# Kernel optimization log

Measured on AMD Instinct MI355X. Metric: run time of the kernel, lower is better.

Reference implementation:

```python
import jax, jax.numpy as jnp
import numpy as np

jax.config.update("jax_enable_x64", True)

P = 2038074743          # prime used by the ROBE-Z hash
BLOCK_K = 32            # tile sizes of the hashed reconstruction (kernel tile)
BLOCK_N = 32
INPUT_DIM = 8192
OUTPUT_DIM = 8192
HASH_SIZE = 1 << 22     # compressed parameter count
TOKENS = 512


def setup_inputs() -> dict:
    key = jax.random.key(0)
    k1, k2 = jax.random.split(key, 2)
    x = jax.random.normal(k1, (TOKENS, INPUT_DIM), dtype=jnp.float32)
    hashed_weight = jax.random.normal(k2, (HASH_SIZE,), dtype=jnp.float32) * 0.02
    bias = jnp.zeros((OUTPUT_DIM,), dtype=jnp.float32)
    # mirrors RzLinear._generate_random_numbers(seed): 4 random ints made even, prepended with P
    rng = np.random.RandomState(1024)
    r = rng.randint(0, P, size=(4,)).astype(np.int64)
    r = r + (r % 2)
    random_numbers = jnp.asarray(np.concatenate([np.array([P], dtype=np.int64), r]), dtype=jnp.int64)
    return {"x": x, "hashed_weight": hashed_weight, "bias": bias, "random_numbers": random_numbers}


def _weight_indices(random_numbers):
    """Hashed flat indices into hashed_weight for the dense [K, N] weight."""
    K, N = INPUT_DIM, OUTPUT_DIM
    kt, nt = K // BLOCK_K, N // BLOCK_N
    R1, R2, R3 = random_numbers[1], random_numbers[2], random_numbers[3]
    k_ids = jnp.arange(kt, dtype=jnp.int64)
    n_ids = jnp.arange(nt, dtype=jnp.int64)
    # per-tile start offset into the compressed array
    start = ((k_ids[:, None] * R3 + n_ids[None, :] * R2 + R1) % P) % (HASH_SIZE - BLOCK_K * BLOCK_N + 1)
    start = start.astype(jnp.int32)  # [kt, nt]
    off = (jnp.arange(BLOCK_K, dtype=jnp.int32)[:, None] * BLOCK_N
           + jnp.arange(BLOCK_N, dtype=jnp.int32)[None, :])  # [BK, BN], row-major within tile
    idx = start[:, None, :, None] + off[None, :, None, :]    # [kt, BK, nt, BN]
    return idx.reshape(K, N)


def reference(x, hashed_weight, bias, random_numbers):
    idx = _weight_indices(random_numbers)          # [K, N] int32
    W = hashed_weight[idx]                          # hashed-gather reconstruction, [K, N]
    out = jnp.matmul(x, W) + bias[None, :]          # [tokens, N]
    return out
```

## Files before the change

### kernel.cpp

```cpp
#include <hip/hip_runtime.h>
#include <hip/hip_fp16.h>

#define NDIM 8192
#define KDIM 8192
#define NT 256
#define MOD2 4193281
#define PRIME 2038074743LL

#define BM 256
#define BN 128
#define BK 32
#define KITER 64
#define BSLAB 1032

typedef _Float16 half8 __attribute__((ext_vector_type(8)));
typedef float floatx4 __attribute__((ext_vector_type(4)));

__global__ __launch_bounds__(256) void prep_kernel(const float* __restrict__ x,
                                                   const float* __restrict__ hw,
                                                   const float* __restrict__ bias,
                                                   const int* __restrict__ rn,
                                                   __half* __restrict__ xh,
                                                   __half* __restrict__ hh,
                                                   int* __restrict__ starts,
                                                   float* __restrict__ out) {
    int b = blockIdx.x;
    int tid = threadIdx.x;
    if (b < 8192) {
        int i = b * 256 + tid;
        const float4* s; __half2* d; int j;
        if (i < (1 << 20)) { s = (const float4*)x;  d = (__half2*)xh; j = i; }
        else               { s = (const float4*)hw; d = (__half2*)hh; j = i - (1 << 20); }
        float4 v = s[j];
        d[j * 2]     = __floats2half2_rn(v.x, v.y);
        d[j * 2 + 1] = __floats2half2_rn(v.z, v.w);
    } else if (b < 8192 + 4096) {
        int i = (b - 8192) * 256 + tid;
        float4 bv = *(const float4*)(bias + ((i & 2047) << 2));
        ((float4*)out)[i] = bv;
    } else {
        int t = (b - 12288) * 256 + tid;
        bool is64 = (rn[1] == 0 && rn[3] == 0);
        long long R1 = is64 ? rn[2] : rn[1];
        long long R2 = is64 ? rn[4] : rn[2];
        long long R3 = is64 ? rn[6] : rn[3];
        long long k_id = t >> 8, n_id = t & 255;
        long long v = (k_id * R3 + n_id * R2 + R1) % PRIME;
        starts[t] = (int)(v % MOD2);
    }
}

__device__ __forceinline__ void gload16(const __half* g, __half* l) {
    __builtin_amdgcn_global_load_lds((const __attribute__((address_space(1))) void*)g,
                                     (__attribute__((address_space(3))) void*)l, 16, 0, 0);
}

#define SBAR() __builtin_amdgcn_sched_barrier(0)
#define WAIT_LGKM0() __builtin_amdgcn_s_waitcnt(0xC07F)

__global__ __launch_bounds__(512, 4) void gemm_kernel(
    const __half* __restrict__ xh, const __half* __restrict__ hh,
    const int* __restrict__ starts, float* __restrict__ out) {
    __shared__ __align__(16) __half As[3][BM * 32];
    __shared__ __align__(16) __half Bs[3][4 * BSLAB];
    __shared__ int Ss[KITER * 4];

    const int tid = threadIdx.x;
    const int lane = tid & 63;
    const int wave = tid >> 6;
    const int wm = wave >> 1;
    const int wn = wave & 1;
    const int quad = lane >> 4;
    const int l16 = lane & 15;

    const int i = blockIdx.x;
    const int ks = i & 3;
    const int m_blk = (i >> 2) & 1;
    const int n_blk = i >> 3;
    const int gm0 = m_blk * BM;
    const int gn0 = n_blk * BN;
    const int kt0 = ks * KITER;
    const int n_id0 = n_blk * 4;

    if (tid < KITER * 4) {
        int kp = tid >> 2, tile = tid & 3;
        Ss[tid] = starts[(kt0 + kp) * NT + n_id0 + tile];
    }

    const int a_t = wave * 2;
    const int a_chunk = (lane & 3) ^ ((lane >> 3) & 3);
    const __half* a_g0 = xh + (size_t)(gm0 + a_t * 16 + (lane >> 2)) * KDIM
                         + kt0 * 32 + a_chunk * 8;
    const __half* a_g1 = a_g0 + (size_t)16 * KDIM;

#define STAGE_A(c_, kp_) do {                                                  \
        gload16(a_g0 + (kp_) * 32, &As[c_][a_t * 512]);                        \
        gload16(a_g1 + (kp_) * 32, &As[c_][a_t * 512 + 512]);                  \
    } while (0)

    const int b_tile = tid >> 7;
    const int t7 = tid & 127;
    const int b_np = t7 & 15;
    const int b_kg = t7 >> 4;
    const int b_oct = b_kg >> 1;
    const unsigned b_base = b_oct * BSLAB;
    const unsigned b_pos = (b_tile * 32 + 2 * b_np) * 8 + (b_kg & 1) * 4;
    const unsigned bswz = (b_np & 4) << 1;

    unsigned pbA0, pbA1, pbA2, pbA3, pbB0, pbB1, pbB2, pbB3;

#define LOADT(Q0, Q1, Q2, Q3, kp_) do {                                        \
        int st = Ss[(kp_) * 4 + b_tile];                                       \
        const __half* src = hh + st + b_kg * 128 + b_np * 2;                   \
        Q0 = *(const unsigned*)(src);                                          \
        Q1 = *(const unsigned*)(src + 32);                                     \
        Q2 = *(const unsigned*)(src + 64);                                     \
        Q3 = *(const unsigned*)(src + 96);                                     \
    } while (0)

#define STORET(Q0, Q1, Q2, Q3, c_) do {                                        \
        unsigned lo0 = (Q0 & 0xffffu) | (Q1 << 16);                            \
        unsigned lo1 = (Q2 & 0xffffu) | (Q3 << 16);                            \
        unsigned hi0 = (Q0 >> 16) | (Q1 & 0xffff0000u);                        \
        unsigned hi1 = (Q2 >> 16) | (Q3 & 0xffff0000u);                        \
        uint2 e = {lo0, lo1}, o = {hi0, hi1};                                  \
        *(uint2*)&Bs[c_][b_base + (b_pos ^ bswz)] = e;                         \
        *(uint2*)&Bs[c_][b_base + ((b_pos + 8) ^ bswz)] = o;                   \
    } while (0)

    floatx4 acc[4][4];
#pragma unroll
    for (int r = 0; r < 4; r++)
#pragma unroll
        for (int c = 0; c < 4; c++)
            acc[r][c] = (floatx4){0.f, 0.f, 0.f, 0.f};

    const unsigned rswz = (unsigned)(l16 & 8);
    const unsigned a_rswz = (unsigned)((l16 >> 1) & 3);

    half8 fa0, fa1, fa2, fa3, fb0, fb1, fb2, fb3;

#define READF(c_) do {                                                         \
        fa0 = *(const half8*)&As[c_][(unsigned)(wm * 64 +  0 + l16) * 32 + ((quad ^ a_rswz) * 8)]; \
        fa1 = *(const half8*)&As[c_][(unsigned)(wm * 64 + 16 + l16) * 32 + ((quad ^ a_rswz) * 8)]; \
        fa2 = *(const half8*)&As[c_][(unsigned)(wm * 64 + 32 + l16) * 32 + ((quad ^ a_rswz) * 8)]; \
        fa3 = *(const half8*)&As[c_][(unsigned)(wm * 64 + 48 + l16) * 32 + ((quad ^ a_rswz) * 8)]; \
        fb0 = *(const half8*)&Bs[c_][quad * BSLAB + ((unsigned)((wn * 64 +  0 + l16) * 8) ^ rswz)]; \
        fb1 = *(const half8*)&Bs[c_][quad * BSLAB + ((unsigned)((wn * 64 + 16 + l16) * 8) ^ rswz)]; \
        fb2 = *(const half8*)&Bs[c_][quad * BSLAB + ((unsigned)((wn * 64 + 32 + l16) * 8) ^ rswz)]; \
        fb3 = *(const half8*)&Bs[c_][quad * BSLAB + ((unsigned)((wn * 64 + 48 + l16) * 8) ^ rswz)]; \
    } while (0)

#define MFMAC() do {                                                           \
        __builtin_amdgcn_s_setprio(1);                                         \
        acc[0][0] = __builtin_amdgcn_mfma_f32_16x16x32_f16(fa0, fb0, acc[0][0], 0, 0, 0); \
        acc[1][0] = __builtin_amdgcn_mfma_f32_16x16x32_f16(fa1, fb0, acc[1][0], 0, 0, 0); \
        acc[2][0] = __builtin_amdgcn_mfma_f32_16x16x32_f16(fa2, fb0, acc[2][0], 0, 0, 0); \
        acc[3][0] = __builtin_amdgcn_mfma_f32_16x16x32_f16(fa3, fb0, acc[3][0], 0, 0, 0); \
        acc[0][1] = __builtin_amdgcn_mfma_f32_16x16x32_f16(fa0, fb1, acc[0][1], 0, 0, 0); \
        acc[1][1] = __builtin_amdgcn_mfma_f32_16x16x32_f16(fa1, fb1, acc[1][1], 0, 0, 0); \
        acc[2][1] = __builtin_amdgcn_mfma_f32_16x16x32_f16(fa2, fb1, acc[2][1], 0, 0, 0); \
        acc[3][1] = __builtin_amdgcn_mfma_f32_16x16x32_f16(fa3, fb1, acc[3][1], 0, 0, 0); \
        acc[0][2] = __builtin_amdgcn_mfma_f32_16x16x32_f16(fa0, fb2, acc[0][2], 0, 0, 0); \
        acc[1][2] = __builtin_amdgcn_mfma_f32_16x16x32_f16(fa1, fb2, acc[1][2], 0, 0, 0); \
        acc[2][2] = __builtin_amdgcn_mfma_f32_16x16x32_f16(fa2, fb2, acc[2][2], 0, 0, 0); \
        acc[3][2] = __builtin_amdgcn_mfma_f32_16x16x32_f16(fa3, fb2, acc[3][2], 0, 0, 0); \
        acc[0][3] = __builtin_amdgcn_mfma_f32_16x16x32_f16(fa0, fb3, acc[0][3], 0, 0, 0); \
        acc[1][3] = __builtin_amdgcn_mfma_f32_16x16x32_f16(fa1, fb3, acc[1][3], 0, 0, 0); \
        acc[2][3] = __builtin_amdgcn_mfma_f32_16x16x32_f16(fa2, fb3, acc[2][3], 0, 0, 0); \
        acc[3][3] = __builtin_amdgcn_mfma_f32_16x16x32_f16(fa3, fb3, acc[3][3], 0, 0, 0); \
        __builtin_amdgcn_s_setprio(0);                                         \
    } while (0)

    unsigned ca = 0, cb = 1, cc = 2, ct;
#define ROT() do { ct = ca; ca = cb; cb = cc; cc = ct; } while (0)

    __syncthreads();
    STAGE_A(0, 0);
    SBAR();
    LOADT(pbA0, pbA1, pbA2, pbA3, 0);
    STAGE_A(1, 1);
    SBAR();
    LOADT(pbB0, pbB1, pbB2, pbB3, 1);
    STORET(pbA0, pbA1, pbA2, pbA3, 0);
    __syncthreads();

    for (int kp = 0; kp < KITER; kp += 2) {
        READF(ca);
        if (kp + 2 < KITER) {
            STAGE_A(cc, kp + 2);
            SBAR();
            LOADT(pbA0, pbA1, pbA2, pbA3, kp + 2);
        }
        SBAR();
        __builtin_amdgcn_s_barrier();
        SBAR();
        MFMAC();
        STORET(pbB0, pbB1, pbB2, pbB3, cb);
        SBAR();
        WAIT_LGKM0();
        __builtin_amdgcn_s_barrier();
        SBAR();
        ROT();

        READF(ca);
        if (kp + 3 < KITER) {
            STAGE_A(cc, kp + 3);
            SBAR();
            LOADT(pbB0, pbB1, pbB2, pbB3, kp + 3);
        }
        SBAR();
        __builtin_amdgcn_s_barrier();
        SBAR();
        MFMAC();
        if (kp + 2 < KITER)
            STORET(pbA0, pbA1, pbA2, pbA3, cb);
        SBAR();
        WAIT_LGKM0();
        __builtin_amdgcn_s_barrier();
        SBAR();
        ROT();
    }

#pragma unroll
    for (int c = 0; c < 4; c++) {
        int col = gn0 + wn * 64 + c * 16 + l16;
#pragma unroll
        for (int r = 0; r < 4; r++) {
            int row0 = gm0 + wm * 64 + r * 16 + quad * 4;
#pragma unroll
            for (int e = 0; e < 4; e++)
                atomicAdd(&out[(size_t)(row0 + e) * NDIM + col], acc[r][c][e]);
        }
    }
#undef LOADT
#undef STORET
#undef READF
#undef MFMAC
#undef STAGE_A
#undef ROT
}

extern "C" void kernel_launch(void* const* d_in, const int* in_sizes, int n_in,
                              void* d_out, int out_size, void* d_ws, size_t ws_size,
                              hipStream_t stream) {
    const float* x = (const float*)d_in[0];
    const float* hw = (const float*)d_in[1];
    const float* bias = (const float*)d_in[2];
    const int* rn = (const int*)d_in[3];
    float* out = (float*)d_out;

    char* ws = (char*)d_ws;
    __half* xh = (__half*)ws;
    __half* hh = (__half*)(ws + (8u << 20));
    int* starts = (int*)(ws + (16u << 20));

    hipLaunchKernelGGL(prep_kernel, dim3(12544), dim3(256), 0, stream,
                       x, hw, bias, rn, xh, hh, starts, out);
    hipLaunchKernelGGL(gemm_kernel, dim3(512), dim3(512), 0, stream, xh, hh, starts, out);
}
```

Before: 195.7 us.

## Deepen GEMM K-loop pipeline to one barrier per stage with static buffer indices

Reworks the main K loop from a rotating triple-buffer with two barriers per step into an unrolled six-phase schedule. Each phase reads fragments from one LDS buffer, stages A and loads B tiles further ahead, waits once on LDS, barriers once, then issues the MFMAs and stores the B tile. A prologue and explicit epilogue are added. The goal is to halve barrier count and keep more global loads in flight. The cost is longer register lifetimes, more code, and tighter correctness requirements on hazards between buffers.

```diff
diff --git a/kernel.cpp b/kernel.cpp
--- a/kernel.cpp
+++ b/kernel.cpp
@@ -172,55 +172,63 @@
         __builtin_amdgcn_s_setprio(0);                                         \
     } while (0)
 
-    unsigned ca = 0, cb = 1, cc = 2, ct;
-#define ROT() do { ct = ca; ca = cb; cb = cc; cc = ct; } while (0)
+#define PHASE(bR, bS, QL0,QL1,QL2,QL3, QS0,QS1,QS2,QS3, t_) do {               \
+        READF(bR);                                                             \
+        STAGE_A(bS, (t_) + 2);                                                 \
+        SBAR();                                                                \
+        LOADT(QL0,QL1,QL2,QL3, (t_) + 3);                                      \
+        SBAR();                                                                \
+        WAIT_LGKM0();                                                          \
+        __builtin_amdgcn_s_barrier();                                          \
+        SBAR();                                                                \
+        MFMAC();                                                               \
+        STORET(QS0,QS1,QS2,QS3, bS);                                           \
+        SBAR();                                                                \
+    } while (0)
 
     __syncthreads();
     STAGE_A(0, 0);
+    STAGE_A(1, 1);
     SBAR();
     LOADT(pbA0, pbA1, pbA2, pbA3, 0);
-    STAGE_A(1, 1);
-    SBAR();
     LOADT(pbB0, pbB1, pbB2, pbB3, 1);
     STORET(pbA0, pbA1, pbA2, pbA3, 0);
+    SBAR();
+    LOADT(pbA0, pbA1, pbA2, pbA3, 2);
+    STORET(pbB0, pbB1, pbB2, pbB3, 1);
     __syncthreads();
 
-    for (int kp = 0; kp < KITER; kp += 2) {
-        READF(ca);
-        if (kp + 2 < KITER) {
-            STAGE_A(cc, kp + 2);
-            SBAR();
-            LOADT(pbA0, pbA1, pbA2, pbA3, kp + 2);
-        }
-        SBAR();
-        __builtin_amdgcn_s_barrier();
-        SBAR();
-        MFMAC();
-        STORET(pbB0, pbB1, pbB2, pbB3, cb);
-        SBAR();
-        WAIT_LGKM0();
-        __builtin_amdgcn_s_barrier();
-        SBAR();
-        ROT();
-
-        READF(ca);
-        if (kp + 3 < KITER) {
-            STAGE_A(cc, kp + 3);
-            SBAR();
-            LOADT(pbB0, pbB1, pbB2, pbB3, kp + 3);
-        }
-        SBAR();
-        __builtin_amdgcn_s_barrier();
-        SBAR();
-        MFMAC();
-        if (kp + 2 < KITER)
-            STORET(pbA0, pbA1, pbA2, pbA3, cb);
-        SBAR();
-        WAIT_LGKM0();
-        __builtin_amdgcn_s_barrier();
-        SBAR();
-        ROT();
-    }
+    for (int t = 0; t < 60; t += 6) {
+        PHASE(0, 2, pbB0,pbB1,pbB2,pbB3, pbA0,pbA1,pbA2,pbA3, t + 0);
+        PHASE(1, 0, pbA0,pbA1,pbA2,pbA3, pbB0,pbB1,pbB2,pbB3, t + 1);
+        PHASE(2, 1, pbB0,pbB1,pbB2,pbB3, pbA0,pbA1,pbA2,pbA3, t + 2);
+        PHASE(0, 2, pbA0,pbA1,pbA2,pbA3, pbB0,pbB1,pbB2,pbB3, t + 3);
+        PHASE(1, 0, pbB0,pbB1,pbB2,pbB3, pbA0,pbA1,pbA2,pbA3, t + 4);
+        PHASE(2, 1, pbA0,pbA1,pbA2,pbA3, pbB0,pbB1,pbB2,pbB3, t + 5);
+    }
+
+    PHASE(0, 2, pbB0,pbB1,pbB2,pbB3, pbA0,pbA1,pbA2,pbA3, 60);
+    READF(1);
+    STAGE_A(0, 63);
+    SBAR();
+    WAIT_LGKM0();
+    __builtin_amdgcn_s_barrier();
+    SBAR();
+    MFMAC();
+    STORET(pbB0, pbB1, pbB2, pbB3, 0);
+    SBAR();
+    READF(2);
+    SBAR();
+    __builtin_amdgcn_s_waitcnt(0x0070);
+    __builtin_amdgcn_s_barrier();
+    SBAR();
+    MFMAC();
+    READF(0);
+    SBAR();
+    WAIT_LGKM0();
+    __builtin_amdgcn_s_barrier();
+    SBAR();
+    MFMAC();
 
 #pragma unroll
     for (int c = 0; c < 4; c++) {
@@ -238,7 +246,7 @@
 #undef READF
 #undef MFMAC
 #undef STAGE_A
-#undef ROT
+#undef PHASE
 }
 
 extern "C" void kernel_launch(void* const* d_in, const int* in_sizes, int n_in,
```

After: 196.8 us. No clear change (+0.6%).
